# Optimization experiments

Measured on AMD Instinct MI355X. Metric: run time of the kernel, lower is better.

## Reference

```python
import jax, jax.numpy as jnp
import numpy as np
import math

N_HEADS = 16
D_EFF = 64
ROPE_BASE = 500.0


def _rope(x, cos, sin):
    # x: (b, h, L, d_eff); cos/sin: (L, d_eff//2)
    x_even = x[..., 0::2]
    x_odd = x[..., 1::2]
    rot = jnp.stack([x_even * cos - x_odd * sin,
                     x_even * sin + x_odd * cos], axis=-1)
    return rot.reshape(x.shape)


def setup_inputs() -> dict:
    key = jax.random.key(0)
    ks = jax.random.split(key, 5)
    B, L, D = 1, 2048, 1024
    X = jax.random.normal(ks[0], (B, L, D), dtype=jnp.float32)
    # causal mask (1 = keep, 0 = masked), broadcastable to (B, h, L, L)
    mask = jnp.tril(jnp.ones((L, L), dtype=jnp.int32))[None, :, :]
    s = 1.0 / math.sqrt(D)
    Wq = jax.random.normal(ks[1], (D, D), dtype=jnp.float32) * s
    Wk = jax.random.normal(ks[2], (D, D), dtype=jnp.float32) * s
    Wv = jax.random.normal(ks[3], (D, D), dtype=jnp.float32) * s
    Wo = jax.random.normal(ks[4], (D, D), dtype=jnp.float32) * s
    return {"X": X, "mask": mask, "Wq": Wq, "Wk": Wk, "Wv": Wv, "Wo": Wo}


def reference(X, mask, Wq, Wk, Wv, Wo):
    b, L, d_model = X.shape
    h, d = N_HEADS, D_EFF
    d_full = h * d

    def split_heads(Y):
        return Y.reshape(b, L, h, d).transpose(0, 2, 1, 3)  # (b,h,L,d)

    Q = split_heads(X @ Wq)
    K = split_heads(X @ Wk)
    V = split_heads(X @ Wv)

    # interleaved RoPE, base 500
    inv_freq = 1.0 / (ROPE_BASE ** (jnp.arange(0, d, 2, dtype=jnp.float32) / d))
    freqs = jnp.arange(L, dtype=jnp.float32)[:, None] * inv_freq  # (L, d/2)
    cos, sin = jnp.cos(freqs), jnp.sin(freqs)
    Q = _rope(Q, cos, sin)
    K = _rope(K, cos, sin)

    S = jnp.einsum('bhqd,bhkd->bhqk', Q, K) / math.sqrt(d)
    S = jnp.where(mask[:, None, :, :] == 0, jnp.float32(-1e9), S)
    # NOTE: faithful to original torch code: softmax over the HEADS axis (dim=1)
    A = jax.nn.softmax(S, axis=1)
    Y = jnp.einsum('bhqk,bhkd->bhqd', A, V)
    Y = Y.transpose(0, 2, 1, 3).reshape(b, L, d_full)
    Y = Y @ Wo
    return Y * math.sqrt(d_model / d_full)
```

## Files before the change

kernel.cpp:

```cpp
#include <hip/hip_runtime.h>
#include <stdint.h>
#include <stddef.h>

typedef __attribute__((ext_vector_type(8))) short bf16x8;
typedef __attribute__((ext_vector_type(4))) short short4v;
typedef __attribute__((ext_vector_type(4))) float f32x4;

__device__ __forceinline__ short f2bf(float f) {
  union { float f; uint32_t u; } x; x.f = f;
  return (short)((x.u + 0x7fffu + ((x.u >> 16) & 1u)) >> 16);
}
__device__ __forceinline__ float bf2f(short s) {
  union { uint32_t u; float f; } x; x.u = ((uint32_t)(uint16_t)s) << 16;
  return x.f;
}

__device__ __forceinline__ void gload_lds16(const void* g, void* lds) {
  __builtin_amdgcn_global_load_lds(
      (const __attribute__((address_space(1))) void*)g,
      (__attribute__((address_space(3))) void*)lds, 16, 0, 0);
}

__global__ __launch_bounds__(256) void cast_b(const float* __restrict__ s,
                                              short* __restrict__ d) {
  int i4 = (blockIdx.x * 256 + threadIdx.x) * 4;
  float4 v = *(const float4*)&s[i4];
  short4v r = { f2bf(v.x), f2bf(v.y), f2bf(v.z), f2bf(v.w) };
  *(short4v*)&d[i4] = r;
}

__global__ __launch_bounds__(256) void cast_add4(const short* __restrict__ Y0,
                                                 const short* __restrict__ Y1,
                                                 const short* __restrict__ Y2,
                                                 const short* __restrict__ Y3,
                                                 const float* __restrict__ Cvs,
                                                 short* __restrict__ o) {
  int i4 = (blockIdx.x * 256 + threadIdx.x) * 4;
  short4v a = *(const short4v*)&Y0[i4];
  short4v b = *(const short4v*)&Y1[i4];
  short4v c = *(const short4v*)&Y2[i4];
  short4v d = *(const short4v*)&Y3[i4];
  short4v r;
#pragma unroll
  for (int j = 0; j < 4; j++) {
    float s = bf2f(a[j]) + bf2f(b[j]) + bf2f(c[j]) + bf2f(d[j]) +
              Cvs[(i4 + j) & 1023];
    r[j] = f2bf(s);
  }
  *(short4v*)&o[i4] = r;
}

__global__ __launch_bounds__(256) void transW(const float* __restrict__ Wq,
                                              const float* __restrict__ Wk,
                                              const float* __restrict__ Wv,
                                              const float* __restrict__ Wo,
                                              short* __restrict__ WcatT,
                                              short* __restrict__ WoT) {
  int z = blockIdx.z;
  const float* src = (z == 0) ? Wq : (z == 1) ? Wk : (z == 2) ? Wv : Wo;
  short* dst = (z == 3) ? WoT : WcatT + (size_t)z * 1024 * 1024;
  __shared__ float tl[32][33];
  int tx = threadIdx.x & 31, ty = threadIdx.x >> 5;
  int kk0 = blockIdx.x * 32;
  int nn0 = blockIdx.y * 32;
#pragma unroll
  for (int j = 0; j < 4; j++)
    tl[ty + j * 8][tx] = src[(size_t)(kk0 + ty + j * 8) * 1024 + nn0 + tx];
  __syncthreads();
#pragma unroll
  for (int j = 0; j < 4; j++)
    dst[(size_t)(nn0 + ty + j * 8) * 1024 + kk0 + tx] = f2bf(tl[tx][ty + j * 8]);
}

__global__ __launch_bounds__(256) void transpose_v(const short* __restrict__ Vb,
                                                   short* __restrict__ Vt) {
  __shared__ short tv[64][72];
  int h = blockIdx.y, k0 = blockIdx.x * 64;
  int tid = threadIdx.x;
#pragma unroll
  for (int j = 0; j < 2; j++) {
    int idx = tid + j * 256;
    int row = idx >> 3, c = idx & 7;
    bf16x8 v = *(const bf16x8*)&Vb[((size_t)h * 2048 + k0 + row) * 64 + c * 8];
#pragma unroll
    for (int t = 0; t < 8; t++) tv[row][c * 8 + t] = v[t];
  }
  __syncthreads();
#pragma unroll
  for (int j = 0; j < 2; j++) {
    int idx = tid + j * 256;
    int d = idx >> 3, c = idx & 7;
    bf16x8 v;
#pragma unroll
    for (int t = 0; t < 8; t++) v[t] = tv[c * 8 + t][d];
    *(bf16x8*)&Vt[((size_t)h * 64 + d) * 2048 + k0 + c * 8] = v;
  }
}

__global__ __launch_bounds__(256) void vsum(const short* __restrict__ Vb,
                                            float* __restrict__ Cvs) {
  __shared__ float red[16][17];
  int h = blockIdx.x >> 2, dq = blockIdx.x & 3;
  int dl = threadIdx.x & 15, ks = threadIdx.x >> 4;
  int d = dq * 16 + dl;
  float acc = 0.f;
  const short* base = &Vb[((size_t)h * 2048 + ks * 128) * 64 + d];
#pragma unroll 8
  for (int k = 0; k < 128; k++) acc += bf2f(base[(size_t)k * 64]);
  red[dl][ks] = acc;
  __syncthreads();
  if (threadIdx.x < 16) {
    float sum = 0.f;
#pragma unroll
    for (int i = 0; i < 16; i++) sum += red[threadIdx.x][i];
    Cvs[h * 64 + dq * 16 + threadIdx.x] = sum * 0.0625f;
  }
}

template <int MODE>
__global__ __launch_bounds__(256, 2)
void gemm_kernel(const short* __restrict__ A, const short* __restrict__ B,
                 int N, int K, float* __restrict__ C,
                 short* __restrict__ Qb, short* __restrict__ Kb,
                 short* __restrict__ Vb) {
  __shared__ __attribute__((aligned(16))) short lga[128 * 64];
  __shared__ __attribute__((aligned(16))) short lgb[128 * 64];
  const int tid = threadIdx.x;
  const int lane = tid & 63;
  const int w = tid >> 6;
  const int l15 = lane & 15;
  const int quad = lane >> 4;
  const int wm = w >> 1, wn = w & 1;
  const int m0 = blockIdx.x * 128, n0 = blockIdx.y * 128;
  const int rsub = lane >> 3;
  const int cpos = lane & 7;

  f32x4 acc[4][4];
#pragma unroll
  for (int i = 0; i < 4; i++)
#pragma unroll
    for (int j = 0; j < 4; j++) acc[i][j] = (f32x4){0.f, 0.f, 0.f, 0.f};

  for (int kb = 0; kb < K; kb += 64) {
    __syncthreads();
#pragma unroll
    for (int j = 0; j < 4; j++) {
      int r = (w * 4 + j) * 8 + rsub;
      int kc = cpos ^ rsub;
      gload_lds16(A + (size_t)(m0 + r) * K + kb + kc * 8, &lga[(w * 4 + j) * 512]);
      gload_lds16(B + (size_t)(n0 + r) * K + kb + kc * 8, &lgb[(w * 4 + j) * 512]);
    }
    __syncthreads();
#pragma unroll
    for (int kk = 0; kk < 2; kk++) {
      bf16x8 af[4], bfr[4];
#pragma unroll
      for (int t = 0; t < 4; t++) {
        int row = wm * 64 + t * 16 + l15;
        int pc = (kk * 4 + quad) ^ (row & 7);
        af[t] = *(const bf16x8*)&lga[row * 64 + pc * 8];
        int rowb = wn * 64 + t * 16 + l15;
        int pcb = (kk * 4 + quad) ^ (rowb & 7);
        bfr[t] = *(const bf16x8*)&lgb[rowb * 64 + pcb * 8];
      }
#pragma unroll
      for (int mt = 0; mt < 4; mt++)
#pragma unroll
        for (int nt = 0; nt < 4; nt++)
          acc[mt][nt] = __builtin_amdgcn_mfma_f32_16x16x32_bf16(
              af[mt], bfr[nt], acc[mt][nt], 0, 0, 0);
    }
  }

  if (MODE == 0) {
#pragma unroll
    for (int mt = 0; mt < 4; mt++) {
      int q = m0 + wm * 64 + mt * 16 + quad * 4;
#pragma unroll
      for (int nt = 0; nt < 4; nt++) {
        int n = n0 + wn * 64 + nt * 16 + l15;
#pragma unroll
        for (int r = 0; r < 4; r++) C[(size_t)(q + r) * N + n] = acc[mt][nt][r];
      }
    }
  } else {
#pragma unroll
    for (int mt = 0; mt < 4; mt++) {
#pragma unroll
      for (int nt = 0; nt < 4; nt++) {
        int n = n0 + wn * 64 + nt * 16 + l15;
        int mat = n >> 10;
        int h = (n >> 6) & 15;
        int d = n & 63;
#pragma unroll
        for (int r = 0; r < 4; r++) {
          int q = m0 + wm * 64 + mt * 16 + quad * 4 + r;
          float v = acc[mt][nt][r];
          float o = __shfl_xor(v, 1, 64);
          if (mat < 2) {
            int i = d >> 1;
            float ang = (float)q * __builtin_exp2f(-(float)i * 0.2801807588956902f);
            float sn, cs;
            __sincosf(ang, &sn, &cs);
            float rv = (d & 1) ? (o * sn + v * cs) : (v * cs - o * sn);
            short* dst = (mat == 0) ? Qb : Kb;
            dst[((size_t)h * 2048 + q) * 64 + d] = f2bf(rv);
          } else {
            Vb[((size_t)h * 2048 + q) * 64 + d] = f2bf(v);
          }
        }
      }
    }
  }
}

__global__ __launch_bounds__(512, 4)
void attn_kernel(const short* __restrict__ Qb, const short* __restrict__ Kb,
                 const short* __restrict__ Vt, short* __restrict__ Yp) {
  __shared__ short Sb[16 * 16 * 72];
  __shared__ short Ab[16 * 16 * 72];
  const int tid = threadIdx.x;
  const int lane = tid & 63;
  const int w = tid >> 6;
  const int l15 = lane & 15, quad = lane >> 4;
  const int bx = blockIdx.x;
  const int qt = 127 - (bx >> 2);
  const int s = bx & 3;
  const int q0 = qt * 16;
  const int G = (qt + 4) >> 2;
  const int h0 = w * 2;

  bf16x8 qf[2][2];
#pragma unroll
  for (int hh = 0; hh < 2; hh++)
#pragma unroll
    for (int c = 0; c < 2; c++)
      qf[hh][c] = *(const bf16x8*)&Qb[((size_t)(h0 + hh) * 2048 + q0 + l15) * 64 +
                                      c * 32 + quad * 8];

  f32x4 yacc[2][4];
#pragma unroll
  for (int i = 0; i < 2; i++)
#pragma unroll
    for (int j = 0; j < 4; j++) yacc[i][j] = (f32x4){0.f, 0.f, 0.f, 0.f};

  for (int g = s; g < G; g += 4) {
    const int k0 = g * 64;
#pragma unroll
    for (int hh = 0; hh < 2; hh++) {
      int h = h0 + hh;
#pragma unroll
      for (int st = 0; st < 4; st++) {
        const short* kb = &Kb[((size_t)h * 2048 + k0 + st * 16 + l15) * 64 + quad * 8];
        bf16x8 kf0 = *(const bf16x8*)kb;
        bf16x8 kf1 = *(const bf16x8*)(kb + 32);
        f32x4 sa = (f32x4){0.f, 0.f, 0.f, 0.f};
        sa = __builtin_amdgcn_mfma_f32_16x16x32_bf16(qf[hh][0], kf0, sa, 0, 0, 0);
        sa = __builtin_amdgcn_mfma_f32_16x16x32_bf16(qf[hh][1], kf1, sa, 0, 0, 0);
#pragma unroll
        for (int r = 0; r < 4; r++)
          Sb[(h * 16 + quad * 4 + r) * 72 + st * 16 + l15] = f2bf(0.125f * sa[r]);
      }
    }
    __syncthreads();
#pragma unroll
    for (int pp = 0; pp < 2; pp++) {
      int p = tid + pp * 512;
      int q = p >> 6, kl = p & 63;
      int base = q * 72 + kl;
      float t[16];
      float m = -1e30f;
#pragma unroll
      for (int h = 0; h < 16; h++) {
        t[h] = bf2f(Sb[h * 1152 + base]);
        m = fmaxf(m, t[h]);
      }
      float sum = 0.f;
#pragma unroll
      for (int h = 0; h < 16; h++) {
        float e = __expf(t[h] - m);
        t[h] = e;
        sum += e;
      }
      float rs = 1.f / sum;
      bool msk = (k0 + kl) > (q0 + q);
#pragma unroll
      for (int h = 0; h < 16; h++)
        Ab[h * 1152 + base] = msk ? (short)0 : f2bf(t[h] * rs - 0.0625f);
    }
    __syncthreads();
#pragma unroll
    for (int hh = 0; hh < 2; hh++) {
      int h = h0 + hh;
#pragma unroll
      for (int kk = 0; kk < 2; kk++) {
        bf16x8 af = *(const bf16x8*)&Ab[(h * 16 + l15) * 72 + kk * 32 + quad * 8];
#pragma unroll
        for (int nt = 0; nt < 4; nt++) {
          bf16x8 vf = *(const bf16x8*)&Vt[((size_t)h * 64 + nt * 16 + l15) * 2048 +
                                          k0 + kk * 32 + quad * 8];
          yacc[hh][nt] = __builtin_amdgcn_mfma_f32_16x16x32_bf16(af, vf, yacc[hh][nt],
                                                                 0, 0, 0);
        }
      }
    }
    __syncthreads();
  }
  short* Y = Yp + (size_t)s * 2048 * 1024;
#pragma unroll
  for (int hh = 0; hh < 2; hh++) {
#pragma unroll
    for (int nt = 0; nt < 4; nt++) {
      int col = (h0 + hh) * 64 + nt * 16 + l15;
#pragma unroll
      for (int r = 0; r < 4; r++)
        Y[(size_t)(q0 + quad * 4 + r) * 1024 + col] = f2bf(yacc[hh][nt][r]);
    }
  }
}

extern "C" void kernel_launch(void* const* d_in, const int* in_sizes, int n_in,
                              void* d_out, int out_size, void* d_ws, size_t ws_size,
                              hipStream_t stream) {
  (void)in_sizes; (void)n_in; (void)out_size; (void)ws_size;
  const float* X  = (const float*)d_in[0];
  const float* Wq = (const float*)d_in[2];
  const float* Wk = (const float*)d_in[3];
  const float* Wv = (const float*)d_in[4];
  const float* Wo = (const float*)d_in[5];
  char* ws = (char*)d_ws;
  const size_t MB = 1024 * 1024;
  short* Xbf   = (short*)(ws + 0);
  short* WcatT = (short*)(ws + 4 * MB);
  short* WoT   = (short*)(ws + 10 * MB);
  short* Qb    = (short*)(ws + 12 * MB);
  short* Kb    = (short*)(ws + 16 * MB);
  short* Vb    = (short*)(ws + 20 * MB);
  short* Vt    = (short*)(ws + 24 * MB);
  short* Yp    = (short*)(ws + 28 * MB);
  float* Cvs   = (float*)(ws + 44 * MB);
  short* Ycbf  = Xbf;
  float* out   = (float*)d_out;

  cast_b<<<dim3(2048), dim3(256), 0, stream>>>(X, Xbf);
  transW<<<dim3(32, 32, 4), dim3(256), 0, stream>>>(Wq, Wk, Wv, Wo, WcatT, WoT);
  gemm_kernel<1><<<dim3(16, 24), dim3(256), 0, stream>>>(Xbf, WcatT, 3072, 1024,
                                                         nullptr, Qb, Kb, Vb);
  transpose_v<<<dim3(32, 16), dim3(256), 0, stream>>>(Vb, Vt);
  vsum<<<dim3(64), dim3(256), 0, stream>>>(Vb, Cvs);
  attn_kernel<<<dim3(512), dim3(512), 0, stream>>>(Qb, Kb, Vt, Yp);
  cast_add4<<<dim3(2048), dim3(256), 0, stream>>>(Yp, Yp + 2048 * 1024,
                                                  Yp + 2 * 2048 * 1024,
                                                  Yp + 3 * 2048 * 1024, Cvs, Ycbf);
  gemm_kernel<0><<<dim3(16, 8), dim3(256), 0, stream>>>(Ycbf, WoT, 1024, 1024,
                                                        out, nullptr, nullptr, nullptr);
}
```

Baseline: 237.3 us.

## Split attention key loop eight ways, reuse score LDS buffer, use packed bf16 converts

Attention work is split over eight key-chunk partitions instead of four, doubling the grid to 1024 blocks. The reduction kernel now sums eight partial bf16 outputs, and the workspace layout grows to hold them. The separate probability LDS buffer is dropped in favour of writing in place into the score buffer, which halves LDS per block and permits a higher occupancy hint. Scores are prescaled by log2(e) so softmax can use exp2, and float-to-bf16 conversion uses the packed hardware instruction. The cost is more partial-sum memory traffic and more work in the final reduction.

Result: slower. 249.0 us (+4.9%).

```diff
diff --git a/kernel.cpp b/kernel.cpp
--- a/kernel.cpp
+++ b/kernel.cpp
@@ -13,6 +13,11 @@
 __device__ __forceinline__ float bf2f(short s) {
   union { uint32_t u; float f; } x; x.u = ((uint32_t)(uint16_t)s) << 16;
   return x.f;
+}
+__device__ __forceinline__ uint32_t cvt_pk_bf16(float a, float b) {
+  uint32_t r;
+  asm("v_cvt_pk_bf16_f32 %0, %1, %2" : "=v"(r) : "v"(a), "v"(b));
+  return r;
 }
 
 __device__ __forceinline__ void gload_lds16(const void* g, void* lds) {
@@ -29,24 +34,22 @@
   *(short4v*)&d[i4] = r;
 }
 
-__global__ __launch_bounds__(256) void cast_add4(const short* __restrict__ Y0,
-                                                 const short* __restrict__ Y1,
-                                                 const short* __restrict__ Y2,
-                                                 const short* __restrict__ Y3,
+__global__ __launch_bounds__(256) void cast_add8(const short* __restrict__ Yp,
                                                  const float* __restrict__ Cvs,
                                                  short* __restrict__ o) {
   int i4 = (blockIdx.x * 256 + threadIdx.x) * 4;
-  short4v a = *(const short4v*)&Y0[i4];
-  short4v b = *(const short4v*)&Y1[i4];
-  short4v c = *(const short4v*)&Y2[i4];
-  short4v d = *(const short4v*)&Y3[i4];
-  short4v r;
-#pragma unroll
-  for (int j = 0; j < 4; j++) {
-    float s = bf2f(a[j]) + bf2f(b[j]) + bf2f(c[j]) + bf2f(d[j]) +
-              Cvs[(i4 + j) & 1023];
-    r[j] = f2bf(s);
-  }
+  float a0 = Cvs[(i4 + 0) & 1023];
+  float a1 = Cvs[(i4 + 1) & 1023];
+  float a2 = Cvs[(i4 + 2) & 1023];
+  float a3 = Cvs[(i4 + 3) & 1023];
+#pragma unroll
+  for (int p = 0; p < 8; p++) {
+    short4v a = *(const short4v*)&Yp[(size_t)p * (2048 * 1024) + i4];
+    a0 += bf2f(a[0]); a1 += bf2f(a[1]); a2 += bf2f(a[2]); a3 += bf2f(a[3]);
+  }
+  uint32_t u0 = cvt_pk_bf16(a0, a1);
+  uint32_t u1 = cvt_pk_bf16(a2, a3);
+  short4v r = { (short)u0, (short)(u0 >> 16), (short)u1, (short)(u1 >> 16) };
   *(short4v*)&o[i4] = r;
 }
 
@@ -214,18 +217,17 @@
   }
 }
 
-__global__ __launch_bounds__(512, 4)
+__global__ __launch_bounds__(512, 8)
 void attn_kernel(const short* __restrict__ Qb, const short* __restrict__ Kb,
                  const short* __restrict__ Vt, short* __restrict__ Yp) {
   __shared__ short Sb[16 * 16 * 72];
-  __shared__ short Ab[16 * 16 * 72];
   const int tid = threadIdx.x;
   const int lane = tid & 63;
   const int w = tid >> 6;
   const int l15 = lane & 15, quad = lane >> 4;
   const int bx = blockIdx.x;
-  const int qt = 127 - (bx >> 2);
-  const int s = bx & 3;
+  const int qt = 127 - (bx >> 3);
+  const int s = bx & 7;
   const int q0 = qt * 16;
   const int G = (qt + 4) >> 2;
   const int h0 = w * 2;
@@ -244,7 +246,7 @@
 #pragma unroll
     for (int j = 0; j < 4; j++) yacc[i][j] = (f32x4){0.f, 0.f, 0.f, 0.f};
 
-  for (int g = s; g < G; g += 4) {
+  for (int g = s; g < G; g += 8) {
     const int k0 = g * 64;
 #pragma unroll
     for (int hh = 0; hh < 2; hh++) {
@@ -257,9 +259,14 @@
         f32x4 sa = (f32x4){0.f, 0.f, 0.f, 0.f};
         sa = __builtin_amdgcn_mfma_f32_16x16x32_bf16(qf[hh][0], kf0, sa, 0, 0, 0);
         sa = __builtin_amdgcn_mfma_f32_16x16x32_bf16(qf[hh][1], kf1, sa, 0, 0, 0);
-#pragma unroll
-        for (int r = 0; r < 4; r++)
-          Sb[(h * 16 + quad * 4 + r) * 72 + st * 16 + l15] = f2bf(0.125f * sa[r]);
+        const float cs = 0.18033688011112042f;
+        uint32_t u0 = cvt_pk_bf16(sa[0] * cs, sa[1] * cs);
+        uint32_t u1 = cvt_pk_bf16(sa[2] * cs, sa[3] * cs);
+        int rb = (h * 16 + quad * 4) * 72 + st * 16 + l15;
+        Sb[rb]       = (short)u0;
+        Sb[rb + 72]  = (short)(u0 >> 16);
+        Sb[rb + 144] = (short)u1;
+        Sb[rb + 216] = (short)(u1 >> 16);
       }
     }
     __syncthreads();
@@ -278,15 +285,19 @@
       float sum = 0.f;
 #pragma unroll
       for (int h = 0; h < 16; h++) {
-        float e = __expf(t[h] - m);
+        float e = __builtin_exp2f(t[h] - m);
         t[h] = e;
         sum += e;
       }
-      float rs = 1.f / sum;
       bool msk = (k0 + kl) > (q0 + q);
-#pragma unroll
-      for (int h = 0; h < 16; h++)
-        Ab[h * 1152 + base] = msk ? (short)0 : f2bf(t[h] * rs - 0.0625f);
+      float rs = msk ? 0.f : 1.f / sum;
+      float off = msk ? 0.f : 0.0625f;
+#pragma unroll
+      for (int h = 0; h < 16; h += 2) {
+        uint32_t u = cvt_pk_bf16(t[h] * rs - off, t[h + 1] * rs - off);
+        Sb[h * 1152 + base]       = (short)u;
+        Sb[(h + 1) * 1152 + base] = (short)(u >> 16);
+      }
     }
     __syncthreads();
 #pragma unroll
@@ -294,7 +305,7 @@
       int h = h0 + hh;
 #pragma unroll
       for (int kk = 0; kk < 2; kk++) {
-        bf16x8 af = *(const bf16x8*)&Ab[(h * 16 + l15) * 72 + kk * 32 + quad * 8];
+        bf16x8 af = *(const bf16x8*)&Sb[(h * 16 + l15) * 72 + kk * 32 + quad * 8];
 #pragma unroll
         for (int nt = 0; nt < 4; nt++) {
           bf16x8 vf = *(const bf16x8*)&Vt[((size_t)h * 64 + nt * 16 + l15) * 2048 +
@@ -338,7 +349,7 @@
   short* Vb    = (short*)(ws + 20 * MB);
   short* Vt    = (short*)(ws + 24 * MB);
   short* Yp    = (short*)(ws + 28 * MB);
-  float* Cvs   = (float*)(ws + 44 * MB);
+  float* Cvs   = (float*)(ws + 60 * MB);
   short* Ycbf  = Xbf;
   float* out   = (float*)d_out;
 
@@ -348,10 +359,8 @@
                                                          nullptr, Qb, Kb, Vb);
   transpose_v<<<dim3(32, 16), dim3(256), 0, stream>>>(Vb, Vt);
   vsum<<<dim3(64), dim3(256), 0, stream>>>(Vb, Cvs);
-  attn_kernel<<<dim3(512), dim3(512), 0, stream>>>(Qb, Kb, Vt, Yp);
-  cast_add4<<<dim3(2048), dim3(256), 0, stream>>>(Yp, Yp + 2048 * 1024,
-                                                  Yp + 2 * 2048 * 1024,
-                                                  Yp + 3 * 2048 * 1024, Cvs, Ycbf);
+  attn_kernel<<<dim3(1024), dim3(512), 0, stream>>>(Qb, Kb, Vt, Yp);
+  cast_add8<<<dim3(2048), dim3(256), 0, stream>>>(Yp, Cvs, Ycbf);
   gemm_kernel<0><<<dim3(16, 8), dim3(256), 0, stream>>>(Ycbf, WoT, 1024, 1024,
                                                         out, nullptr, nullptr, nullptr);
 }
```
